# Optimization experiments

Hardware: AMD Instinct MI355X
Metric: run time of the kernel (lower is better)

The kernel has to match this reference:

```python
import jax, jax.numpy as jnp
import numpy as np

B, T, C = 2, 2048, 768
H = 12
D = C // H
HID = 4 * C
EPS = 1e-5
LS_INIT = 1e-4


def _ln(x, g, b):
    mu = jnp.mean(x, axis=-1, keepdims=True)
    var = jnp.mean((x - mu) ** 2, axis=-1, keepdims=True)
    return (x - mu) * jax.lax.rsqrt(var + EPS) * g + b


def setup_inputs() -> dict:
    key = jax.random.key(0)
    ks = jax.random.split(key, 10)
    s = lambda fan_in: 1.0 / np.sqrt(fan_in)
    return {
        "x": jax.random.normal(ks[0], (B, T, C), dtype=jnp.float32),
        "mask_logits": jnp.zeros((B, 1, T, T), dtype=jnp.float32),
        "bias": jax.random.normal(ks[1], (B, H, T, T), dtype=jnp.float32),
        "ln1_g": jnp.ones((C,), jnp.float32),
        "ln1_b": jnp.zeros((C,), jnp.float32),
        "qkv_w": jax.random.normal(ks[2], (3 * C, C), jnp.float32) * s(C),
        "qkv_b": jnp.zeros((3 * C,), jnp.float32),
        "proj_w": jax.random.normal(ks[3], (C, C), jnp.float32) * s(C),
        "proj_b": jnp.zeros((C,), jnp.float32),
        "ls1": jnp.full((C,), LS_INIT, jnp.float32),
        "ln2_g": jnp.ones((C,), jnp.float32),
        "ln2_b": jnp.zeros((C,), jnp.float32),
        "w1": jax.random.normal(ks[4], (HID, C), jnp.float32) * s(C),
        "b1": jnp.zeros((HID,), jnp.float32),
        "w2": jax.random.normal(ks[5], (C, HID), jnp.float32) * s(HID),
        "b2": jnp.zeros((C,), jnp.float32),
        "ls2": jnp.full((C,), LS_INIT, jnp.float32),
    }


def reference(x, mask_logits, bias, ln1_g, ln1_b, qkv_w, qkv_b, proj_w, proj_b,
              ls1, ln2_g, ln2_b, w1, b1, w2, b2, ls2):
    scale = 1.0 / np.sqrt(D)
    xn = _ln(x, ln1_g, ln1_b)
    qkv = xn @ qkv_w.T + qkv_b                      # [B,T,3C]
    qkv = qkv.reshape(B, T, 3, H, D).transpose(2, 0, 3, 1, 4)  # [3,B,H,T,D]
    q, k, v = qkv[0], qkv[1], qkv[2]
    logits = jnp.einsum('bhqd,bhkd->bhqk', q, k) * scale + bias + mask_logits
    attn = jax.nn.softmax(logits, axis=-1)          # [B,H,T,T]
    y = jnp.einsum('bhqk,bhkd->bhqd', attn, v)      # [B,H,T,D]
    y = y.transpose(0, 2, 1, 3).reshape(B, T, C)
    y = y @ proj_w.T + proj_b
    x = x + y * ls1
    h = _ln(x, ln2_g, ln2_b)
    h = jax.nn.gelu(h @ w1.T + b1, approximate=False)
    h = h @ w2.T + b2
    x = x + h * ls2
    return x, jax.lax.stop_gradient(attn)
```

## Files before the change

kernel.cpp:

```cpp
#include <hip/hip_runtime.h>
#include <hip/hip_bf16.h>
#include <math.h>

#define B_ 2
#define T_ 2048
#define C_ 768
#define H_ 12
#define D_ 64
#define HID_ 3072
#define NROW 4096
#define N3C 2304

typedef short bf16x8 __attribute__((ext_vector_type(8)));
typedef float f32x4 __attribute__((ext_vector_type(4)));
typedef unsigned short u16;
typedef unsigned int u32;

__device__ inline u16 f2bf(float f) {
    u32 u = __float_as_uint(f);
    u32 r = (u + 0x7fffu + ((u >> 16) & 1u)) >> 16;
    return (u16)r;
}

__device__ __forceinline__ void dma16(const float* g, float* lds) {
    __builtin_amdgcn_global_load_lds(
        (const __attribute__((address_space(1))) void*)g,
        (__attribute__((address_space(3))) void*)lds, 16, 0, 0);
}

__global__ __launch_bounds__(256) void cvt_bf16_kernel(const float* __restrict__ s,
                                                       u16* __restrict__ d, int n) {
    int i = (blockIdx.x * 256 + threadIdx.x) * 4;
    if (i >= n) return;
    float4 v = *(const float4*)(s + i);
    ushort4 o;
    o.x = f2bf(v.x); o.y = f2bf(v.y); o.z = f2bf(v.z); o.w = f2bf(v.w);
    *(ushort4*)(d + i) = o;
}

__global__ __launch_bounds__(256) void ln_kernel(const float* __restrict__ x,
                                                 const float* __restrict__ g,
                                                 const float* __restrict__ b,
                                                 u16* __restrict__ out) {
    int row = blockIdx.x, t = threadIdx.x;
    const float* xr = x + (size_t)row * C_;
    float v[3], s = 0.f, sq = 0.f;
#pragma unroll
    for (int i = 0; i < 3; i++) {
        v[i] = xr[i * 256 + t];
        s += v[i]; sq += v[i] * v[i];
    }
    for (int m = 32; m; m >>= 1) { s += __shfl_xor(s, m); sq += __shfl_xor(sq, m); }
    __shared__ float ss[4], ssq[4];
    int wid = t >> 6;
    if ((t & 63) == 0) { ss[wid] = s; ssq[wid] = sq; }
    __syncthreads();
    s = ss[0] + ss[1] + ss[2] + ss[3];
    sq = ssq[0] + ssq[1] + ssq[2] + ssq[3];
    float mu = s * (1.f / C_);
    float var = sq * (1.f / C_) - mu * mu;
    float rstd = rsqrtf(var + 1e-5f);
#pragma unroll
    for (int i = 0; i < 3; i++) {
        int c = i * 256 + t;
        out[(size_t)row * C_ + c] = f2bf((v[i] - mu) * rstd * g[c] + b[c]);
    }
}

template <int EPI>
__global__ __launch_bounds__(256) void gemm_kernel(const u16* __restrict__ A,
                                                   const u16* __restrict__ W,
                                                   const float* __restrict__ bias,
                                                   float* __restrict__ outf,
                                                   u16* __restrict__ outb,
                                                   const float* __restrict__ res,
                                                   const float* __restrict__ ls,
                                                   int N, int K) {
    __shared__ u16 Alds[128 * 64];
    __shared__ u16 Blds[128 * 64];
    int tid = threadIdx.x;
    int m0 = blockIdx.y * 128, n0 = blockIdx.x * 128;
    int lane = tid & 63, wid = tid >> 6;
    int wr = wid >> 1, wc = wid & 1;
    int lr = lane & 15, lq = lane >> 4;

    f32x4 acc[4][4];
#pragma unroll
    for (int i = 0; i < 4; i++)
#pragma unroll
        for (int j = 0; j < 4; j++) acc[i][j] = (f32x4){0.f, 0.f, 0.f, 0.f};

    int nk = K >> 6;
    const u16* Ab = A + (size_t)m0 * K;
    const u16* Wb = W + (size_t)n0 * K;
    bf16x8 ra[4], rb[4];
#pragma unroll
    for (int i = 0; i < 4; i++) {
        int c = tid + i * 256, row = c >> 3, j = c & 7;
        ra[i] = *(const bf16x8*)(Ab + (size_t)row * K + j * 8);
        rb[i] = *(const bf16x8*)(Wb + (size_t)row * K + j * 8);
    }
    for (int kt = 0; kt < nk; ++kt) {
        __syncthreads();
#pragma unroll
        for (int i = 0; i < 4; i++) {
            int c = tid + i * 256, row = c >> 3, j = c & 7;
            int off = row * 64 + ((j ^ (row & 7)) << 3);
            *(bf16x8*)(Alds + off) = ra[i];
            *(bf16x8*)(Blds + off) = rb[i];
        }
        __syncthreads();
        if (kt + 1 < nk) {
            int k0 = (kt + 1) << 6;
#pragma unroll
            for (int i = 0; i < 4; i++) {
                int c = tid + i * 256, row = c >> 3, j = c & 7;
                ra[i] = *(const bf16x8*)(Ab + (size_t)row * K + k0 + j * 8);
                rb[i] = *(const bf16x8*)(Wb + (size_t)row * K + k0 + j * 8);
            }
        }
#pragma unroll
        for (int s = 0; s < 2; s++) {
            bf16x8 af[4], bw[4];
#pragma unroll
            for (int i = 0; i < 4; i++) {
                int arow = wr * 64 + i * 16 + lr;
                af[i] = *(const bf16x8*)(Alds + arow * 64 + (((4 * s + lq) ^ (arow & 7)) << 3));
                int brow = wc * 64 + i * 16 + lr;
                bw[i] = *(const bf16x8*)(Blds + brow * 64 + (((4 * s + lq) ^ (brow & 7)) << 3));
            }
#pragma unroll
            for (int i = 0; i < 4; i++)
#pragma unroll
                for (int j = 0; j < 4; j++)
                    acc[i][j] = __builtin_amdgcn_mfma_f32_16x16x32_bf16(af[i], bw[j], acc[i][j], 0, 0, 0);
        }
    }
#pragma unroll
    for (int i = 0; i < 4; i++) {
#pragma unroll
        for (int j = 0; j < 4; j++) {
#pragma unroll
            for (int r = 0; r < 4; r++) {
                int gm = m0 + wr * 64 + i * 16 + lq * 4 + r;
                int gn = n0 + wc * 64 + j * 16 + lr;
                float val = acc[i][j][r] + bias[gn];
                if (EPI == 0) {
                    outb[(size_t)gm * N + gn] = f2bf(val);
                } else if (EPI == 1) {
                    float gl = 0.5f * val * (1.f + erff(val * 0.70710678118654752f));
                    outb[(size_t)gm * N + gn] = f2bf(gl);
                } else {
                    outf[(size_t)gm * N + gn] = res[(size_t)gm * N + gn] + ls[gn] * val;
                }
            }
        }
    }
}

__global__ __launch_bounds__(256) void vtrans_kernel(const u16* __restrict__ qkv,
                                                     u16* __restrict__ vt) {
    __shared__ u16 tile[64 * 72];
    int t0 = blockIdx.x * 64, h = blockIdx.y, b = blockIdx.z;
    int tid = threadIdx.x;
#pragma unroll
    for (int i = 0; i < 2; i++) {
        int c = tid + i * 256, tr = c >> 3, j = c & 7;
        bf16x8 v = *(const bf16x8*)(qkv + (size_t)(b * T_ + t0 + tr) * N3C + 1536 + h * 64 + j * 8);
        *(bf16x8*)(tile + tr * 72 + j * 8) = v;
    }
    __syncthreads();
#pragma unroll
    for (int i = 0; i < 2; i++) {
        int c = tid + i * 256, d = c >> 3, tj = c & 7;
        bf16x8 o;
#pragma unroll
        for (int k = 0; k < 8; k++) o[k] = (short)tile[(tj * 8 + k) * 72 + d];
        *(bf16x8*)(vt + (size_t)((b * H_ + h) * 64 + d) * T_ + t0 + tj * 8) = o;
    }
}

__global__ __launch_bounds__(256, 2) void attn_kernel(const u16* __restrict__ qkv,
                                                      const u16* __restrict__ vt,
                                                      const float* __restrict__ bias,
                                                      const float* __restrict__ mask,
                                                      float* __restrict__ attn_out,
                                                      u16* __restrict__ ybuf) {
    __shared__ u16 S[16 * 2048];
    __shared__ float stg[4][2][2][256];
    char* Sb = (char*)S;
    int qt = blockIdx.x, h = blockIdx.y, b = blockIdx.z;
    int tid = threadIdx.x, lane = tid & 63, wid = tid >> 6;
    int lr = lane & 15, lq = lane >> 4;
    int q0 = qt * 16;
    size_t bh = (size_t)(b * H_ + h);
    const float scale = 0.125f;

    const u16* qp = qkv + (size_t)(b * T_ + q0 + lr) * N3C + h * 64;
    bf16x8 qa0 = *(const bf16x8*)(qp + lq * 8);
    bf16x8 qa1 = *(const bf16x8*)(qp + 32 + lq * 8);
    const u16* kbase = qkv + (size_t)(b * T_ + wid * 512 + lr) * N3C + 768 + h * 64 + lq * 8;
#pragma unroll 4
    for (int ct = 0; ct < 32; ++ct) {
        bf16x8 kf0 = *(const bf16x8*)(kbase + (size_t)ct * 16 * N3C);
        bf16x8 kf1 = *(const bf16x8*)(kbase + (size_t)ct * 16 * N3C + 32);
        f32x4 a = (f32x4){0.f, 0.f, 0.f, 0.f};
        a = __builtin_amdgcn_mfma_f32_16x16x32_bf16(kf0, qa0, a, 0, 0, 0);
        a = __builtin_amdgcn_mfma_f32_16x16x32_bf16(kf1, qa1, a, 0, 0, 0);
        int colbase = wid * 512 + ct * 16;
        ushort4 pk;
        pk.x = f2bf(a[0] * scale);
        pk.y = f2bf(a[1] * scale);
        pk.z = f2bf(a[2] * scale);
        pk.w = f2bf(a[3] * scale);
        *(ushort4*)(Sb + (((u32)lr * 4096 + 2 * colbase + 8 * lq) ^ ((lr & 7) << 4))) = pk;
    }
    __syncthreads();

    const float* bias_base = bias + (bh * T_ + q0 + wid * 4) * T_;
    const float* mask_base = mask + ((size_t)b * T_ + q0 + wid * 4) * T_;
    float lsum4[4] = {0.f, 0.f, 0.f, 0.f};

    dma16(bias_base + lane * 4, &stg[wid][0][0][0]);
    dma16(bias_base + (size_t)T_ + lane * 4, &stg[wid][0][1][0]);

#pragma unroll 1
    for (int step = 0; step < 16; ++step) {
        int par = step & 1, pr = step >> 3, ch = step & 7;
        asm volatile("s_waitcnt vmcnt(0)" ::: "memory");
        __builtin_amdgcn_sched_barrier(0);
        if (step < 15) {
            int ns = step + 1, npar = ns & 1, npr = ns >> 3, nch = ns & 7;
            const float* g0 = bias_base + (size_t)(2 * npr) * T_ + nch * 256 + lane * 4;
            const float* g1 = bias_base + (size_t)(2 * npr + 1) * T_ + nch * 256 + lane * 4;
            dma16(g0, &stg[wid][npar][0][0]);
            dma16(g1, &stg[wid][npar][1][0]);
        }
        int col = ch * 256 + lane * 4;
        float4 m0 = *(const float4*)(mask_base + (size_t)(2 * pr) * T_ + col);
        float4 m1 = *(const float4*)(mask_base + (size_t)(2 * pr + 1) * T_ + col);
        float4 b0 = *(const float4*)&stg[wid][par][0][lane * 4];
        float4 b1 = *(const float4*)&stg[wid][par][1][lane * 4];
#pragma unroll
        for (int rr = 0; rr < 2; ++rr) {
            int r = wid * 4 + 2 * pr + rr;
            float4 bv = rr ? b1 : b0;
            float4 mv = rr ? m1 : m0;
            u32 addr = ((u32)r * 4096 + (u32)col * 2) ^ ((u32)(r & 7) << 4);
            uint2 s2 = *(const uint2*)(Sb + addr);
            float e0 = __expf(__uint_as_float(s2.x << 16) + bv.x + mv.x);
            float e1 = __expf(__uint_as_float(s2.x & 0xffff0000u) + bv.y + mv.y);
            float e2 = __expf(__uint_as_float(s2.y << 16) + bv.z + mv.z);
            float e3 = __expf(__uint_as_float(s2.y & 0xffff0000u) + bv.w + mv.w);
            lsum4[2 * pr + rr] += (e0 + e1) + (e2 + e3);
            uint2 o;
            o.x = ((u32)f2bf(e1) << 16) | (u32)f2bf(e0);
            o.y = ((u32)f2bf(e3) << 16) | (u32)f2bf(e2);
            *(uint2*)(Sb + addr) = o;
        }
    }
    float rinv_r[4];
#pragma unroll
    for (int rr = 0; rr < 4; ++rr) {
        float ls = lsum4[rr];
        for (int m = 32; m; m >>= 1) ls += __shfl_xor(ls, m);
        rinv_r[rr] = 1.f / ls;
        if (lane == 0) stg[wid][0][0][rr] = rinv_r[rr];
    }
    __syncthreads();

    float* ao_base = attn_out + (bh * T_ + q0 + wid * 4) * T_;
#pragma unroll
    for (int ch = 0; ch < 8; ++ch) {
        int col = ch * 256 + lane * 4;
#pragma unroll
        for (int rr = 0; rr < 4; ++rr) {
            int r = wid * 4 + rr;
            u32 addr = ((u32)r * 4096 + (u32)col * 2) ^ ((u32)(r & 7) << 4);
            uint2 s2 = *(const uint2*)(Sb + addr);
            float rv = rinv_r[rr];
            float4 o;
            o.x = __uint_as_float(s2.x << 16) * rv;
            o.y = __uint_as_float(s2.x & 0xffff0000u) * rv;
            o.z = __uint_as_float(s2.y << 16) * rv;
            o.w = __uint_as_float(s2.y & 0xffff0000u) * rv;
            *(float4*)(ao_base + (size_t)rr * T_ + col) = o;
        }
    }

    f32x4 acc = (f32x4){0.f, 0.f, 0.f, 0.f};
    const u16* vtp = vt + (bh * 64 + wid * 16 + lr) * (size_t)T_ + lq * 8;
#pragma unroll 4
    for (int ks = 0; ks < 64; ++ks) {
        bf16x8 pf = *(const bf16x8*)(Sb + (((u32)lr * 4096 + ks * 64 + lq * 16) ^ ((lr & 7) << 4)));
        bf16x8 vf = *(const bf16x8*)(vtp + ks * 32);
        acc = __builtin_amdgcn_mfma_f32_16x16x32_bf16(pf, vf, acc, 0, 0, 0);
    }
#pragma unroll
    for (int r = 0; r < 4; r++) {
        int row = lq * 4 + r;
        float y = acc[r] * stg[row >> 2][0][0][row & 3];
        ybuf[(size_t)(b * T_ + q0 + row) * C_ + h * 64 + wid * 16 + lr] = f2bf(y);
    }
}

extern "C" void kernel_launch(void* const* d_in, const int* in_sizes, int n_in,
                              void* d_out, int out_size, void* d_ws, size_t ws_size,
                              hipStream_t stream) {
    const float* x = (const float*)d_in[0];
    const float* mask = (const float*)d_in[1];
    const float* bias = (const float*)d_in[2];
    const float* ln1g = (const float*)d_in[3];
    const float* ln1b = (const float*)d_in[4];
    const float* qkvw = (const float*)d_in[5];
    const float* qkvb = (const float*)d_in[6];
    const float* projw = (const float*)d_in[7];
    const float* projb = (const float*)d_in[8];
    const float* ls1 = (const float*)d_in[9];
    const float* ln2g = (const float*)d_in[10];
    const float* ln2b = (const float*)d_in[11];
    const float* w1 = (const float*)d_in[12];
    const float* b1 = (const float*)d_in[13];
    const float* w2 = (const float*)d_in[14];
    const float* b2 = (const float*)d_in[15];
    const float* ls2 = (const float*)d_in[16];

    char* ws = (char*)d_ws;
    size_t off = 0;
    u16* qkvw_b = (u16*)(ws + off); off += (size_t)N3C * C_ * 2;
    u16* projw_b = (u16*)(ws + off); off += (size_t)C_ * C_ * 2;
    u16* w1_b = (u16*)(ws + off); off += (size_t)HID_ * C_ * 2;
    u16* w2_b = (u16*)(ws + off); off += (size_t)C_ * HID_ * 2;
    u16* xn = (u16*)(ws + off); off += (size_t)NROW * C_ * 2;
    u16* qkvbuf = (u16*)(ws + off); off += (size_t)NROW * N3C * 2;
    u16* vt = (u16*)(ws + off); off += (size_t)B_ * H_ * D_ * T_ * 2;
    u16* g = qkvbuf;
    u16* ybuf = (u16*)(ws + off); off += (size_t)NROW * C_ * 2;
    float* x1 = (float*)(ws + off); off += (size_t)NROW * C_ * 4;
    (void)ws_size; (void)n_in; (void)in_sizes; (void)out_size;

    float* outx = (float*)d_out;
    float* attn_out = outx + (size_t)NROW * C_;

    cvt_bf16_kernel<<<(N3C * C_ / 4 + 255) / 256, 256, 0, stream>>>(qkvw, qkvw_b, N3C * C_);
    cvt_bf16_kernel<<<(C_ * C_ / 4 + 255) / 256, 256, 0, stream>>>(projw, projw_b, C_ * C_);
    cvt_bf16_kernel<<<(HID_ * C_ / 4 + 255) / 256, 256, 0, stream>>>(w1, w1_b, HID_ * C_);
    cvt_bf16_kernel<<<(C_ * HID_ / 4 + 255) / 256, 256, 0, stream>>>(w2, w2_b, C_ * HID_);

    ln_kernel<<<NROW, 256, 0, stream>>>(x, ln1g, ln1b, xn);
    gemm_kernel<0><<<dim3(N3C / 128, NROW / 128), 256, 0, stream>>>(
        xn, qkvw_b, qkvb, nullptr, qkvbuf, nullptr, nullptr, N3C, C_);
    vtrans_kernel<<<dim3(T_ / 64, H_, B_), 256, 0, stream>>>(qkvbuf, vt);
    attn_kernel<<<dim3(T_ / 16, H_, B_), 256, 0, stream>>>(qkvbuf, vt, bias, mask, attn_out, ybuf);
    gemm_kernel<2><<<dim3(C_ / 128, NROW / 128), 256, 0, stream>>>(
        ybuf, projw_b, projb, x1, nullptr, x, ls1, C_, C_);
    ln_kernel<<<NROW, 256, 0, stream>>>(x1, ln2g, ln2b, xn);
    gemm_kernel<1><<<dim3(HID_ / 128, NROW / 128), 256, 0, stream>>>(
        xn, w1_b, b1, nullptr, g, nullptr, nullptr, HID_, C_);
    gemm_kernel<2><<<dim3(C_ / 128, NROW / 128), 256, 0, stream>>>(
        g, w2_b, b2, outx, nullptr, x1, ls2, C_, HID_);
}
```

Measured before the change: 498.3 us.

## Halve attention query tile to 8 rows and deepen bias/mask DMA prefetch

The attention kernel now handles 8 query rows per block instead of 16, halving the score LDS buffer and doubling the grid. This lets more blocks fit per CU to hide bias/mask streaming. The bias/mask staging moves from a 2-deep bias-only buffer with direct mask loads to a 4-deep ring that DMAs both bias and mask, with explicit vmcnt waits keeping three steps in flight. The cost is that half the MFMA lanes in QK^T and PV are wasted and K/V are re-read twice as often.

```diff
diff --git a/kernel.cpp b/kernel.cpp
--- a/kernel.cpp
+++ b/kernel.cpp
@@ -186,17 +186,17 @@
                                                       const float* __restrict__ mask,
                                                       float* __restrict__ attn_out,
                                                       u16* __restrict__ ybuf) {
-    __shared__ u16 S[16 * 2048];
-    __shared__ float stg[4][2][2][256];
+    __shared__ u16 S[8 * 2048];
+    __shared__ __align__(16) float stg[4][4][2][256];
     char* Sb = (char*)S;
     int qt = blockIdx.x, h = blockIdx.y, b = blockIdx.z;
     int tid = threadIdx.x, lane = tid & 63, wid = tid >> 6;
     int lr = lane & 15, lq = lane >> 4;
-    int q0 = qt * 16;
+    int q0 = qt * 8;
     size_t bh = (size_t)(b * H_ + h);
     const float scale = 0.125f;
 
-    const u16* qp = qkv + (size_t)(b * T_ + q0 + lr) * N3C + h * 64;
+    const u16* qp = qkv + (size_t)(b * T_ + q0 + (lr & 7)) * N3C + h * 64;
     bf16x8 qa0 = *(const bf16x8*)(qp + lq * 8);
     bf16x8 qa1 = *(const bf16x8*)(qp + 32 + lq * 8);
     const u16* kbase = qkv + (size_t)(b * T_ + wid * 512 + lr) * N3C + 768 + h * 64 + lq * 8;
@@ -208,74 +208,75 @@
         a = __builtin_amdgcn_mfma_f32_16x16x32_bf16(kf0, qa0, a, 0, 0, 0);
         a = __builtin_amdgcn_mfma_f32_16x16x32_bf16(kf1, qa1, a, 0, 0, 0);
         int colbase = wid * 512 + ct * 16;
-        ushort4 pk;
-        pk.x = f2bf(a[0] * scale);
-        pk.y = f2bf(a[1] * scale);
-        pk.z = f2bf(a[2] * scale);
-        pk.w = f2bf(a[3] * scale);
-        *(ushort4*)(Sb + (((u32)lr * 4096 + 2 * colbase + 8 * lq) ^ ((lr & 7) << 4))) = pk;
+        if (lr < 8) {
+            ushort4 pk;
+            pk.x = f2bf(a[0] * scale);
+            pk.y = f2bf(a[1] * scale);
+            pk.z = f2bf(a[2] * scale);
+            pk.w = f2bf(a[3] * scale);
+            *(ushort4*)(Sb + (((u32)lr * 4096 + 2 * colbase + 8 * lq) ^ ((lr & 7) << 4))) = pk;
+        }
     }
     __syncthreads();
 
-    const float* bias_base = bias + (bh * T_ + q0 + wid * 4) * T_;
-    const float* mask_base = mask + ((size_t)b * T_ + q0 + wid * 4) * T_;
-    float lsum4[4] = {0.f, 0.f, 0.f, 0.f};
-
-    dma16(bias_base + lane * 4, &stg[wid][0][0][0]);
-    dma16(bias_base + (size_t)T_ + lane * 4, &stg[wid][0][1][0]);
+    const float* bias_base = bias + (bh * T_ + q0 + wid * 2) * T_;
+    const float* mask_base = mask + ((size_t)b * T_ + q0 + wid * 2) * T_;
+    float lsum2[2] = {0.f, 0.f};
+
+#pragma unroll
+    for (int s = 0; s < 3; ++s) {
+        int rl = s >> 3, ch = s & 7;
+        dma16(bias_base + (size_t)rl * T_ + ch * 256 + lane * 4, &stg[wid][s & 3][0][0]);
+        dma16(mask_base + (size_t)rl * T_ + ch * 256 + lane * 4, &stg[wid][s & 3][1][0]);
+    }
 
 #pragma unroll 1
     for (int step = 0; step < 16; ++step) {
-        int par = step & 1, pr = step >> 3, ch = step & 7;
-        asm volatile("s_waitcnt vmcnt(0)" ::: "memory");
+        if (step + 3 < 16) {
+            int ns = step + 3, rl = ns >> 3, ch = ns & 7;
+            dma16(bias_base + (size_t)rl * T_ + ch * 256 + lane * 4, &stg[wid][ns & 3][0][0]);
+            dma16(mask_base + (size_t)rl * T_ + ch * 256 + lane * 4, &stg[wid][ns & 3][1][0]);
+        }
+        if (step < 13)      asm volatile("s_waitcnt vmcnt(6)" ::: "memory");
+        else if (step == 13) asm volatile("s_waitcnt vmcnt(4)" ::: "memory");
+        else if (step == 14) asm volatile("s_waitcnt vmcnt(2)" ::: "memory");
+        else                 asm volatile("s_waitcnt vmcnt(0)" ::: "memory");
         __builtin_amdgcn_sched_barrier(0);
-        if (step < 15) {
-            int ns = step + 1, npar = ns & 1, npr = ns >> 3, nch = ns & 7;
-            const float* g0 = bias_base + (size_t)(2 * npr) * T_ + nch * 256 + lane * 4;
-            const float* g1 = bias_base + (size_t)(2 * npr + 1) * T_ + nch * 256 + lane * 4;
-            dma16(g0, &stg[wid][npar][0][0]);
-            dma16(g1, &stg[wid][npar][1][0]);
-        }
+
+        int rl = step >> 3, ch = step & 7;
+        int r = wid * 2 + rl;
         int col = ch * 256 + lane * 4;
-        float4 m0 = *(const float4*)(mask_base + (size_t)(2 * pr) * T_ + col);
-        float4 m1 = *(const float4*)(mask_base + (size_t)(2 * pr + 1) * T_ + col);
-        float4 b0 = *(const float4*)&stg[wid][par][0][lane * 4];
-        float4 b1 = *(const float4*)&stg[wid][par][1][lane * 4];
-#pragma unroll
-        for (int rr = 0; rr < 2; ++rr) {
-            int r = wid * 4 + 2 * pr + rr;
-            float4 bv = rr ? b1 : b0;
-            float4 mv = rr ? m1 : m0;
-            u32 addr = ((u32)r * 4096 + (u32)col * 2) ^ ((u32)(r & 7) << 4);
-            uint2 s2 = *(const uint2*)(Sb + addr);
-            float e0 = __expf(__uint_as_float(s2.x << 16) + bv.x + mv.x);
-            float e1 = __expf(__uint_as_float(s2.x & 0xffff0000u) + bv.y + mv.y);
-            float e2 = __expf(__uint_as_float(s2.y << 16) + bv.z + mv.z);
-            float e3 = __expf(__uint_as_float(s2.y & 0xffff0000u) + bv.w + mv.w);
-            lsum4[2 * pr + rr] += (e0 + e1) + (e2 + e3);
-            uint2 o;
-            o.x = ((u32)f2bf(e1) << 16) | (u32)f2bf(e0);
-            o.y = ((u32)f2bf(e3) << 16) | (u32)f2bf(e2);
-            *(uint2*)(Sb + addr) = o;
-        }
-    }
-    float rinv_r[4];
-#pragma unroll
-    for (int rr = 0; rr < 4; ++rr) {
-        float ls = lsum4[rr];
+        float4 bv = *(const float4*)&stg[wid][step & 3][0][lane * 4];
+        float4 mv = *(const float4*)&stg[wid][step & 3][1][lane * 4];
+        u32 addr = ((u32)r * 4096 + (u32)col * 2) ^ ((u32)(r & 7) << 4);
+        uint2 s2 = *(const uint2*)(Sb + addr);
+        float e0 = __expf(__uint_as_float(s2.x << 16) + bv.x + mv.x);
+        float e1 = __expf(__uint_as_float(s2.x & 0xffff0000u) + bv.y + mv.y);
+        float e2 = __expf(__uint_as_float(s2.y << 16) + bv.z + mv.z);
+        float e3 = __expf(__uint_as_float(s2.y & 0xffff0000u) + bv.w + mv.w);
+        lsum2[rl] += (e0 + e1) + (e2 + e3);
+        uint2 o;
+        o.x = ((u32)f2bf(e1) << 16) | (u32)f2bf(e0);
+        o.y = ((u32)f2bf(e3) << 16) | (u32)f2bf(e2);
+        *(uint2*)(Sb + addr) = o;
+    }
+    float rinv_r[2];
+#pragma unroll
+    for (int rr = 0; rr < 2; ++rr) {
+        float ls = lsum2[rr];
         for (int m = 32; m; m >>= 1) ls += __shfl_xor(ls, m);
         rinv_r[rr] = 1.f / ls;
         if (lane == 0) stg[wid][0][0][rr] = rinv_r[rr];
     }
     __syncthreads();
 
-    float* ao_base = attn_out + (bh * T_ + q0 + wid * 4) * T_;
+    float* ao_base = attn_out + (bh * T_ + q0 + wid * 2) * T_;
 #pragma unroll
     for (int ch = 0; ch < 8; ++ch) {
         int col = ch * 256 + lane * 4;
 #pragma unroll
-        for (int rr = 0; rr < 4; ++rr) {
-            int r = wid * 4 + rr;
+        for (int rr = 0; rr < 2; ++rr) {
+            int r = wid * 2 + rr;
             u32 addr = ((u32)r * 4096 + (u32)col * 2) ^ ((u32)(r & 7) << 4);
             uint2 s2 = *(const uint2*)(Sb + addr);
             float rv = rinv_r[rr];
@@ -292,15 +293,17 @@
     const u16* vtp = vt + (bh * 64 + wid * 16 + lr) * (size_t)T_ + lq * 8;
 #pragma unroll 4
     for (int ks = 0; ks < 64; ++ks) {
-        bf16x8 pf = *(const bf16x8*)(Sb + (((u32)lr * 4096 + ks * 64 + lq * 16) ^ ((lr & 7) << 4)));
+        bf16x8 pf = *(const bf16x8*)(Sb + (((u32)(lr & 7) * 4096 + ks * 64 + lq * 16) ^ ((u32)(lr & 7) << 4)));
         bf16x8 vf = *(const bf16x8*)(vtp + ks * 32);
         acc = __builtin_amdgcn_mfma_f32_16x16x32_bf16(pf, vf, acc, 0, 0, 0);
     }
 #pragma unroll
     for (int r = 0; r < 4; r++) {
         int row = lq * 4 + r;
-        float y = acc[r] * stg[row >> 2][0][0][row & 3];
-        ybuf[(size_t)(b * T_ + q0 + row) * C_ + h * 64 + wid * 16 + lr] = f2bf(y);
+        if (row < 8) {
+            float y = acc[r] * stg[row >> 1][0][0][row & 1];
+            ybuf[(size_t)(b * T_ + q0 + row) * C_ + h * 64 + wid * 16 + lr] = f2bf(y);
+        }
     }
 }
 
@@ -351,7 +354,7 @@
     gemm_kernel<0><<<dim3(N3C / 128, NROW / 128), 256, 0, stream>>>(
         xn, qkvw_b, qkvb, nullptr, qkvbuf, nullptr, nullptr, N3C, C_);
     vtrans_kernel<<<dim3(T_ / 64, H_, B_), 256, 0, stream>>>(qkvbuf, vt);
-    attn_kernel<<<dim3(T_ / 16, H_, B_), 256, 0, stream>>>(qkvbuf, vt, bias, mask, attn_out, ybuf);
+    attn_kernel<<<dim3(T_ / 8, H_, B_), 256, 0, stream>>>(qkvbuf, vt, bias, mask, attn_out, ybuf);
     gemm_kernel<2><<<dim3(C_ / 128, NROW / 128), 256, 0, stream>>>(
         ybuf, projw_b, projb, x1, nullptr, x, ls1, C_, C_);
     ln_kernel<<<NROW, 256, 0, stream>>>(x1, ln2g, ln2b, xn);
```

After: 750.8 us. 50.7% more time.
